# Performance work log

Measured on AMD Instinct MI355X. Metric: run time of the kernel, lower is better.

Reference implementation:

```python
import jax, jax.numpy as jnp
import numpy as np

D_MODEL = 512
N_HEADS = 4
D_HEAD = D_MODEL // N_HEADS
D_FF = 2048
N_LAYERS = 3
IN_DIM = 25
OUT_DIM = 1
PRE = 20          # pre_training_size
SCALE = 10.0      # scaling_factor
EPS = 1e-5


def setup_inputs() -> dict:
    key = jax.random.key(0)
    ks = jax.random.split(key, 20)
    B, S = 4, 2048
    def gn(k, shape, fan_in):
        return jax.random.normal(k, shape, jnp.float32) * (1.0 / np.sqrt(fan_in))
    return {
        "src": jax.random.normal(ks[0], (B, S, IN_DIM), jnp.float32),
        "emb_w": gn(ks[1], (D_MODEL, IN_DIM), IN_DIM),
        "emb_b": jnp.zeros((D_MODEL,), jnp.float32),
        "in_w": gn(ks[2], (N_LAYERS, 3 * D_MODEL, D_MODEL), D_MODEL),
        "in_b": jnp.zeros((N_LAYERS, 3 * D_MODEL), jnp.float32),
        "out_w": gn(ks[3], (N_LAYERS, D_MODEL, D_MODEL), D_MODEL),
        "out_b": jnp.zeros((N_LAYERS, D_MODEL), jnp.float32),
        "ln1_g": jnp.ones((N_LAYERS, D_MODEL), jnp.float32),
        "ln1_b": jnp.zeros((N_LAYERS, D_MODEL), jnp.float32),
        "ln2_g": jnp.ones((N_LAYERS, D_MODEL), jnp.float32),
        "ln2_b": jnp.zeros((N_LAYERS, D_MODEL), jnp.float32),
        "ff1_w": gn(ks[4], (N_LAYERS, D_FF, D_MODEL), D_MODEL),
        "ff1_b": jnp.zeros((N_LAYERS, D_FF), jnp.float32),
        "ff2_w": gn(ks[5], (N_LAYERS, D_MODEL, D_FF), D_FF),
        "ff2_b": jnp.zeros((N_LAYERS, D_MODEL), jnp.float32),
        "dec_w": gn(ks[6], (OUT_DIM, D_MODEL), D_MODEL),
        "dec_b": jnp.zeros((OUT_DIM,), jnp.float32),
    }


def _layer_norm(x, g, b):
    mu = jnp.mean(x, axis=-1, keepdims=True)
    var = jnp.var(x, axis=-1, keepdims=True)
    return (x - mu) * jax.lax.rsqrt(var + EPS) * g + b


def _pos_encoding(seq_len):
    # eval mode: start index 0, no dropout
    pos = jnp.arange(seq_len, dtype=jnp.float32)[:, None]           # [S,1]
    div = jnp.exp(jnp.arange(0, D_MODEL, 2, dtype=jnp.float32) * (-np.log(10000.0) / D_MODEL))  # [D/2]
    ang = pos * div                                                  # [S,D/2]
    return jnp.stack([jnp.sin(ang), jnp.cos(ang)], axis=-1).reshape(seq_len, D_MODEL)


def _causal_mask(seq_len):
    row = jnp.arange(seq_len)[:, None]
    col = jnp.arange(seq_len)[None, :]
    mask = jnp.where(col <= row, 0.0, -jnp.inf).astype(jnp.float32)
    # include_training_period=True: first PRE x PRE block unmasked
    return mask.at[:PRE, :PRE].set(0.0)


def reference(src, emb_w, emb_b, in_w, in_b, out_w, out_b,
              ln1_g, ln1_b, ln2_g, ln2_b, ff1_w, ff1_b, ff2_w, ff2_b,
              dec_w, dec_b):
    B, S, _ = src.shape
    x = src @ emb_w.T + emb_b                    # [B,S,D]
    x = x + _pos_encoding(S)[None]
    mask = _causal_mask(S)                       # [S,S]
    scale = 1.0 / np.sqrt(D_HEAD)
    for l in range(N_LAYERS):
        # --- self-attention (post-norm, eager bmm+softmax+bmm path) ---
        qkv = x @ in_w[l].T + in_b[l]            # [B,S,3D]
        q, k, v = jnp.split(qkv, 3, axis=-1)
        q = q.reshape(B, S, N_HEADS, D_HEAD).transpose(0, 2, 1, 3)
        k = k.reshape(B, S, N_HEADS, D_HEAD).transpose(0, 2, 1, 3)
        v = v.reshape(B, S, N_HEADS, D_HEAD).transpose(0, 2, 1, 3)
        scores = jnp.einsum('bhqd,bhkd->bhqk', q, k) * scale + mask
        attn = jax.nn.softmax(scores, axis=-1)   # [B,H,S,S] (need_weights=True path)
        o = jnp.einsum('bhqk,bhkd->bhqd', attn, v)
        o = o.transpose(0, 2, 1, 3).reshape(B, S, D_MODEL)
        o = o @ out_w[l].T + out_b[l]
        x = _layer_norm(x + o, ln1_g[l], ln1_b[l])
        # --- FFN ---
        h = jax.nn.relu(x @ ff1_w[l].T + ff1_b[l])
        h = h @ ff2_w[l].T + ff2_b[l]
        x = _layer_norm(x + h, ln2_g[l], ln2_b[l])
    out = jnp.tanh(x @ dec_w.T + dec_b) * SCALE  # [B,S,1]
    return out
```

## Files before the change

kernel.cpp:

```cpp
#include <hip/hip_runtime.h>

#define S_LEN 2048
#define DMODEL 512

typedef __attribute__((ext_vector_type(8))) short bf16x8;
typedef __attribute__((ext_vector_type(4))) float f32x4;
typedef __attribute__((ext_vector_type(4))) unsigned short u16x4;
typedef __attribute__((ext_vector_type(8))) unsigned short u16x8;
typedef __attribute__((ext_vector_type(2))) unsigned int u32x2;

__device__ __forceinline__ unsigned short f2bf(float f) {
    unsigned int u = __float_as_uint(f);
    u += 0x7fff + ((u >> 16) & 1);
    return (unsigned short)(u >> 16);
}
__device__ __forceinline__ float bf2f(unsigned short h) {
    return __uint_as_float(((unsigned int)h) << 16);
}
__device__ __forceinline__ void gll16(const void* g, void* l) {
    __builtin_amdgcn_global_load_lds(
        (const __attribute__((address_space(1))) unsigned int*)g,
        (__attribute__((address_space(3))) unsigned int*)l, 16, 0, 0);
}

__global__ __launch_bounds__(256) void conv_all(
    const float4* __restrict__ in_w, const float4* __restrict__ out_w,
    const float4* __restrict__ ff1_w, const float4* __restrict__ ff2_w,
    u16x4* __restrict__ in_wb, u16x4* __restrict__ out_wb,
    u16x4* __restrict__ ff1_wb, u16x4* __restrict__ ff2_wb)
{
    int i = blockIdx.x * 256 + threadIdx.x;
    const float4* src; u16x4* dst; int j;
    if (i < 589824)        { src = in_w;  dst = in_wb;  j = i; }
    else if (i < 786432)   { src = out_w; dst = out_wb; j = i - 589824; }
    else if (i < 1572864)  { src = ff1_w; dst = ff1_wb; j = i - 786432; }
    else                   { src = ff2_w; dst = ff2_wb; j = i - 1572864; }
    float4 v = src[j];
    u16x4 o = { f2bf(v.x), f2bf(v.y), f2bf(v.z), f2bf(v.w) };
    dst[j] = o;
}

__global__ __launch_bounds__(256) void embed_kernel(
    const float* __restrict__ src, const float* __restrict__ ew,
    const float* __restrict__ eb, float* __restrict__ X,
    unsigned short* __restrict__ Xb)
{
    int rid = blockIdx.x;
    int s = rid & (S_LEN - 1);
    int tid = threadIdx.x;
    __shared__ float sr[25];
    if (tid < 25) sr[tid] = src[rid * 25 + tid];
    __syncthreads();
    #pragma unroll
    for (int rep = 0; rep < 2; rep++) {
        int d = tid + rep * 256;
        float a = eb[d];
        #pragma unroll
        for (int k = 0; k < 25; k++) a = fmaf(sr[k], ew[d * 25 + k], a);
        int i2 = d & ~1;
        float div = expf(-(float)i2 * (9.210340371976184f / 512.f));
        float ang = (float)s * div;
        a += (d & 1) ? cosf(ang) : sinf(ang);
        X[(size_t)rid * DMODEL + d] = a;
        Xb[(size_t)rid * DMODEL + d] = f2bf(a);
    }
}

template<int MODE, int BN>
__global__ __launch_bounds__(256) void gemm_bf16(
    const unsigned short* __restrict__ A, int lda,
    const unsigned short* __restrict__ W, int K,
    const float* __restrict__ bias,
    unsigned short* __restrict__ out, int ldc,
    unsigned short* __restrict__ out2)
{
    constexpr int NJ = BN / 32;
    __shared__ __align__(16) unsigned short As[128 * 64];
    __shared__ __align__(16) unsigned short Ws[BN * 64];
    int tid = threadIdx.x;
    int lane = tid & 63, w = tid >> 6;
    int g = lane >> 4, c15 = lane & 15;
    int wm = w >> 1, wn = w & 1;
    int bm, bn;
    if (BN == 64) {
        int raw = blockIdx.x;
        int lid = ((raw & 7) << 6) | (raw >> 3);
        bn = lid & 7; bm = lid >> 3;
    } else {
        bm = blockIdx.y; bn = blockIdx.x;
    }

    f32x4 acc[4][NJ];
    #pragma unroll
    for (int i = 0; i < 4; i++)
        #pragma unroll
        for (int j = 0; j < NJ; j++) acc[i][j] = (f32x4){0.f, 0.f, 0.f, 0.f};

    const int nk = K >> 6;
    for (int kk = 0; kk < nk; kk++) {
        __syncthreads();
        #pragma unroll
        for (int i = 0; i < 4; i++) {
            int chunk = tid + i * 256;
            int r = chunk >> 3, c = chunk & 7;
            int cs = c ^ (r & 7);
            gll16(A + (size_t)(bm * 128 + r) * lda + kk * 64 + cs * 8,
                  (void*)(As + chunk * 8));
        }
        #pragma unroll
        for (int i = 0; i < BN / 32; i++) {
            int chunk = tid + i * 256;
            int r = chunk >> 3, c = chunk & 7;
            int cs = c ^ (r & 7);
            gll16(W + (size_t)(bn * BN + r) * K + kk * 64 + cs * 8,
                  (void*)(Ws + chunk * 8));
        }
        __syncthreads();
        bf16x8 a[4][2], b[NJ][2];
        #pragma unroll
        for (int mi = 0; mi < 4; mi++) {
            int row = wm * 64 + mi * 16 + c15;
            #pragma unroll
            for (int h = 0; h < 2; h++) {
                int ck = (h * 4 + g) ^ (row & 7);
                a[mi][h] = *(const bf16x8*)((const char*)As + row * 128 + ck * 16);
            }
        }
        #pragma unroll
        for (int nj = 0; nj < NJ; nj++) {
            int row = wn * (BN / 2) + nj * 16 + c15;
            #pragma unroll
            for (int h = 0; h < 2; h++) {
                int ck = (h * 4 + g) ^ (row & 7);
                b[nj][h] = *(const bf16x8*)((const char*)Ws + row * 128 + ck * 16);
            }
        }
        __builtin_amdgcn_s_setprio(1);
        #pragma unroll
        for (int h = 0; h < 2; h++)
            #pragma unroll
            for (int mi = 0; mi < 4; mi++)
                #pragma unroll
                for (int nj = 0; nj < NJ; nj++)
                    acc[mi][nj] = __builtin_amdgcn_mfma_f32_16x16x32_bf16(
                        a[mi][h], b[nj][h], acc[mi][nj], 0, 0, 0);
        __builtin_amdgcn_s_setprio(0);
    }
    #pragma unroll
    for (int nj = 0; nj < NJ; nj++) {
        int colb = bn * BN + wn * (BN / 2) + nj * 16;
        float bv = bias[colb + c15];
        #pragma unroll
        for (int mi = 0; mi < 4; mi++) {
            int rowb = bm * 128 + wm * 64 + mi * 16 + g * 4;
            if (MODE == 3 && colb >= 1024) {
                int cv = colb - 1024 + c15;
                int hh = cv >> 7, d = cv & 127;
                int bb = rowb >> 11, t = rowb & (S_LEN - 1);
                u16x4 pk;
                #pragma unroll
                for (int r = 0; r < 4; r++) pk[r] = f2bf(acc[mi][nj][r] + bv);
                *(u16x4*)(out2 + ((size_t)(bb * 4 + hh) * 128 + d) * S_LEN + t) = pk;
            } else {
                #pragma unroll
                for (int r = 0; r < 4; r++) {
                    float v = acc[mi][nj][r] + bv;
                    if (MODE == 2) v = fmaxf(v, 0.f);
                    out[(size_t)(rowb + r) * ldc + colb + c15] = f2bf(v);
                }
            }
        }
    }
}

__global__ __launch_bounds__(256) void flash_attn(
    const unsigned short* __restrict__ QKb,
    const unsigned short* __restrict__ Vt,
    unsigned short* __restrict__ Ob,
    unsigned short* __restrict__ Opart,
    float* __restrict__ Mpart,
    float* __restrict__ Lpart)
{
    __shared__ __align__(16) unsigned short Ks[2][32 * 128];
    __shared__ __align__(16) unsigned short Vts[2][128 * 32];
    __shared__ __align__(16) unsigned short Plds[4][16 * 40];
    const float scale = 0.08838834764831845f;
    int tid = threadIdx.x;
    int lane = tid & 63, w = tid >> 6;
    int g = lane >> 4, c15 = lane & 15;
    int raw = blockIdx.x;
    int lid = (raw & 7) * 96 + (raw >> 3);
    int bh = lid / 48, idx = lid - bh * 48;
    int b = bh >> 2, h = bh & 3;
    int qb, kt0, nkt, split;
    if (idx < 16) { qb = idx; kt0 = 0; nkt = 2 * qb + 2; split = -1; }
    else {
        int s = idx - 16;
        qb = 16 + (s >> 1);
        int j = s & 1;
        kt0 = j * (qb + 1);
        nkt = qb + 1;
        split = bh * 32 + (qb - 16) * 2 + j;
    }

    bf16x8 q[4];
    {
        const unsigned short* qrow =
            QKb + (size_t)(b * S_LEN + qb * 64 + w * 16 + c15) * 1024 + h * 128;
        #pragma unroll
        for (int k0 = 0; k0 < 4; k0++) q[k0] = *(const bf16x8*)(qrow + k0 * 32 + g * 8);
    }
    f32x4 o[8];
    #pragma unroll
    for (int cd = 0; cd < 8; cd++) o[cd] = (f32x4){0.f, 0.f, 0.f, 0.f};
    float m = -3e38f, l = 0.f;

    auto stage = [&](int kt, int bi) {
        #pragma unroll
        for (int i = 0; i < 2; i++) {
            int chunk = tid + i * 256;
            int r = chunk >> 4, c = chunk & 15;
            int cs = (c & 8) | ((c ^ r) & 7);
            gll16(QKb + (size_t)(b * S_LEN + kt * 32 + r) * 1024 + 512 + h * 128 + cs * 8,
                  (void*)(Ks[bi] + chunk * 8));
        }
        #pragma unroll
        for (int i = 0; i < 2; i++) {
            int chunk = tid + i * 256;
            int r = chunk >> 2, c = chunk & 3;
            int cs = (c ^ r) & 3;
            gll16(Vt + ((size_t)(b * 4 + h) * 128 + r) * S_LEN + kt * 32 + cs * 8,
                  (void*)(Vts[bi] + chunk * 8));
        }
    };

    stage(kt0, 0);
    __syncthreads();
    int buf = 0;

    for (int t = 0; t < nkt; t++) {
        int kt = kt0 + t;
        if (t + 1 < nkt) stage(kt + 1, buf ^ 1);
        f32x4 sf[2];
        __builtin_amdgcn_s_setprio(1);
        #pragma unroll
        for (int c = 0; c < 2; c++) {
            sf[c] = (f32x4){0.f, 0.f, 0.f, 0.f};
            int tok16 = c * 16 + c15;
            #pragma unroll
            for (int k0 = 0; k0 < 4; k0++) {
                int ck = k0 * 4 + g;
                int cs = (ck & 8) | ((ck ^ tok16) & 7);
                bf16x8 kf = *(const bf16x8*)((const char*)Ks[buf] + tok16 * 256 + cs * 16);
                sf[c] = __builtin_amdgcn_mfma_f32_16x16x32_bf16(kf, q[k0], sf[c], 0, 0, 0);
            }
        }
        __builtin_amdgcn_s_setprio(0);
        if (kt >= 2 * qb) {
            int qr = qb * 64 + w * 16 + c15;
            #pragma unroll
            for (int c = 0; c < 2; c++)
                #pragma unroll
                for (int r = 0; r < 4; r++) {
                    int tok = kt * 32 + c * 16 + g * 4 + r;
                    bool ok = (tok <= qr) || (qr < 20 && tok < 20);
                    if (!ok) sf[c][r] = -3e38f;
                }
        }
        float t0 = fmaxf(fmaxf(sf[0][0], sf[0][1]), fmaxf(sf[0][2], sf[0][3]));
        float t1 = fmaxf(fmaxf(sf[1][0], sf[1][1]), fmaxf(sf[1][2], sf[1][3]));
        float mt = fmaxf(t0, t1);
        mt = fmaxf(mt, __shfl_xor(mt, 16));
        mt = fmaxf(mt, __shfl_xor(mt, 32));
        bool need = !__all(mt <= m + 90.5f);
        float sc = 1.f;
        if (need) {
            float mn = fmaxf(m, mt);
            sc = __expf((m - mn) * scale);
            m = mn;
        }
        float msc = m * scale;
        #pragma unroll
        for (int c = 0; c < 2; c++)
            #pragma unroll
            for (int r = 0; r < 4; r++)
                sf[c][r] = __expf(fmaf(sf[c][r], scale, -msc));
        float s0 = (sf[0][0] + sf[0][1]) + (sf[0][2] + sf[0][3]);
        float s1 = (sf[1][0] + sf[1][1]) + (sf[1][2] + sf[1][3]);
        float ls = s0 + s1;
        ls += __shfl_xor(ls, 16);
        ls += __shfl_xor(ls, 32);
        if (need) l *= sc;
        l += ls;
        #pragma unroll
        for (int c = 0; c < 2; c++) {
            unsigned int lo = ((unsigned int)f2bf(sf[c][1]) << 16) | f2bf(sf[c][0]);
            unsigned int hi = ((unsigned int)f2bf(sf[c][3]) << 16) | f2bf(sf[c][2]);
            u32x2 pk = {lo, hi};
            *(u32x2*)&Plds[w][c15 * 40 + c * 16 + g * 4] = pk;
        }
        if (need) {
            float r0 = __shfl(sc, g * 4 + 0);
            float r1 = __shfl(sc, g * 4 + 1);
            float r2 = __shfl(sc, g * 4 + 2);
            float r3 = __shfl(sc, g * 4 + 3);
            #pragma unroll
            for (int cd = 0; cd < 8; cd++) {
                o[cd][0] *= r0; o[cd][1] *= r1; o[cd][2] *= r2; o[cd][3] *= r3;
            }
        }
        bf16x8 pa = *(const bf16x8*)((const char*)&Plds[w][0] + c15 * 80 + g * 16);
        __builtin_amdgcn_s_setprio(1);
        #pragma unroll
        for (int cd = 0; cd < 8; cd++) {
            int dv = cd * 16 + c15;
            int cs = (g ^ dv) & 3;
            bf16x8 vf = *(const bf16x8*)((const char*)Vts[buf] + dv * 64 + cs * 16);
            o[cd] = __builtin_amdgcn_mfma_f32_16x16x32_bf16(pa, vf, o[cd], 0, 0, 0);
        }
        __builtin_amdgcn_s_setprio(0);
        __syncthreads();
        buf ^= 1;
    }

    if (split < 0) {
        float li0 = 1.f / __shfl(l, g * 4 + 0);
        float li1 = 1.f / __shfl(l, g * 4 + 1);
        float li2 = 1.f / __shfl(l, g * 4 + 2);
        float li3 = 1.f / __shfl(l, g * 4 + 3);
        size_t obase = (size_t)(b * S_LEN + qb * 64 + w * 16 + g * 4) * 512 + h * 128;
        #pragma unroll
        for (int cd = 0; cd < 8; cd++) {
            Ob[obase + 0 * 512 + cd * 16 + c15] = f2bf(o[cd][0] * li0);
            Ob[obase + 1 * 512 + cd * 16 + c15] = f2bf(o[cd][1] * li1);
            Ob[obase + 2 * 512 + cd * 16 + c15] = f2bf(o[cd][2] * li2);
            Ob[obase + 3 * 512 + cd * 16 + c15] = f2bf(o[cd][3] * li3);
        }
    } else {
        unsigned short* op = Opart + (size_t)split * 8192;
        int rb = w * 16 + g * 4;
        #pragma unroll
        for (int cd = 0; cd < 8; cd++) {
            op[(rb + 0) * 128 + cd * 16 + c15] = f2bf(o[cd][0]);
            op[(rb + 1) * 128 + cd * 16 + c15] = f2bf(o[cd][1]);
            op[(rb + 2) * 128 + cd * 16 + c15] = f2bf(o[cd][2]);
            op[(rb + 3) * 128 + cd * 16 + c15] = f2bf(o[cd][3]);
        }
        if (g == 0) {
            Mpart[split * 64 + w * 16 + c15] = m;
            Lpart[split * 64 + w * 16 + c15] = l;
        }
    }
}

__global__ __launch_bounds__(256) void attn_merge(
    const unsigned short* __restrict__ Opart,
    const float* __restrict__ Mpart, const float* __restrict__ Lpart,
    unsigned short* __restrict__ Ob)
{
    const float scale = 0.08838834764831845f;
    int bid = blockIdx.x;
    int bh = bid >> 4, qe = bid & 15;
    int qb = 16 + qe;
    int b = bh >> 2, h = bh & 3;
    int p0 = bh * 32 + qe * 2;
    int t = threadIdx.x;
    int r = t >> 2, dq = t & 3;
    float m0 = Mpart[p0 * 64 + r], m1 = Mpart[(p0 + 1) * 64 + r];
    float l0 = Lpart[p0 * 64 + r], l1 = Lpart[(p0 + 1) * 64 + r];
    float ms = fmaxf(m0, m1);
    float w0 = __expf((m0 - ms) * scale), w1 = __expf((m1 - ms) * scale);
    float linv = 1.f / (l0 * w0 + l1 * w1);
    w0 *= linv; w1 *= linv;
    const unsigned short* o0 = Opart + (size_t)p0 * 8192 + r * 128 + dq * 32;
    const unsigned short* o1 = o0 + 8192;
    unsigned short* od = Ob + (size_t)(b * S_LEN + qb * 64 + r) * 512 + h * 128 + dq * 32;
    #pragma unroll
    for (int i = 0; i < 4; i++) {
        u16x8 a = *(const u16x8*)(o0 + i * 8);
        u16x8 c = *(const u16x8*)(o1 + i * 8);
        u16x8 d;
        #pragma unroll
        for (int j = 0; j < 8; j++)
            d[j] = f2bf(bf2f(a[j]) * w0 + bf2f(c[j]) * w1);
        *(u16x8*)(od + i * 8) = d;
    }
}

__global__ __launch_bounds__(256) void add_ln_kernel(
    float* __restrict__ X, const unsigned short* __restrict__ D,
    const float* __restrict__ gw, const float* __restrict__ bw,
    unsigned short* __restrict__ Xb)
{
    int row = blockIdx.x;
    int tid = threadIdx.x;
    size_t base = (size_t)row * DMODEL;
    float v0 = X[base + tid] + bf2f(D[base + tid]);
    float v1 = X[base + tid + 256] + bf2f(D[base + tid + 256]);
    float s = v0 + v1;
    float sq = v0 * v0 + v1 * v1;
    #pragma unroll
    for (int off = 32; off > 0; off >>= 1) {
        s  += __shfl_down(s, off);
        sq += __shfl_down(sq, off);
    }
    __shared__ float red[2][4];
    int wv = tid >> 6;
    if ((tid & 63) == 0) { red[0][wv] = s; red[1][wv] = sq; }
    __syncthreads();
    s  = red[0][0] + red[0][1] + red[0][2] + red[0][3];
    sq = red[1][0] + red[1][1] + red[1][2] + red[1][3];
    float mu = s * (1.f / DMODEL);
    float var = sq * (1.f / DMODEL) - mu * mu;
    float rs = rsqrtf(var + 1e-5f);
    float y0 = (v0 - mu) * rs * gw[tid] + bw[tid];
    float y1 = (v1 - mu) * rs * gw[tid + 256] + bw[tid + 256];
    X[base + tid] = y0;
    X[base + tid + 256] = y1;
    Xb[base + tid] = f2bf(y0);
    Xb[base + tid + 256] = f2bf(y1);
}

__global__ __launch_bounds__(256) void decoder_kernel(
    const float* __restrict__ X, const float* __restrict__ w,
    const float* __restrict__ bias, float* __restrict__ out)
{
    int tid = threadIdx.x;
    int lane = tid & 63;
    int row = blockIdx.x * 4 + (tid >> 6);
    float s = 0.f;
    size_t base = (size_t)row * DMODEL;
    #pragma unroll
    for (int i = 0; i < 8; i++) s = fmaf(X[base + lane + i * 64], w[lane + i * 64], s);
    #pragma unroll
    for (int off = 32; off > 0; off >>= 1) s += __shfl_down(s, off);
    if (lane == 0) out[row] = tanhf(s + bias[0]) * 10.0f;
}

extern "C" void kernel_launch(void* const* d_in, const int* in_sizes, int n_in,
                              void* d_out, int out_size, void* d_ws, size_t ws_size,
                              hipStream_t stream)
{
    const float* src   = (const float*)d_in[0];
    const float* emb_w = (const float*)d_in[1];
    const float* emb_b = (const float*)d_in[2];
    const float* in_w  = (const float*)d_in[3];
    const float* in_b  = (const float*)d_in[4];
    const float* out_w = (const float*)d_in[5];
    const float* out_b = (const float*)d_in[6];
    const float* ln1_g = (const float*)d_in[7];
    const float* ln1_b = (const float*)d_in[8];
    const float* ln2_g = (const float*)d_in[9];
    const float* ln2_b = (const float*)d_in[10];
    const float* ff1_w = (const float*)d_in[11];
    const float* ff1_b = (const float*)d_in[12];
    const float* ff2_w = (const float*)d_in[13];
    const float* ff2_b = (const float*)d_in[14];
    const float* dec_w = (const float*)d_in[15];
    const float* dec_b = (const float*)d_in[16];

    char* ws = (char*)d_ws;
    float*          X   = (float*)ws;
    unsigned short* Xb  = (unsigned short*)(ws + (16u << 20));
    unsigned short* Pb  = (unsigned short*)(ws + (24u << 20));
    unsigned short* Ob  = (unsigned short*)(ws + (32u << 20));
    unsigned short* QKb = (unsigned short*)(ws + (40u << 20));
    unsigned short* Vt  = (unsigned short*)(ws + (56u << 20));
    unsigned short* Hb  = (unsigned short*)(ws + (40u << 20));
    unsigned short* Opart = (unsigned short*)(ws + (16u << 20));
    float* Mpart = (float*)(ws + (24u << 20));
    float* Lpart = Mpart + 512 * 64;
    unsigned short* in_wb  = (unsigned short*)(ws + (72u << 20));
    unsigned short* out_wb = in_wb  + 3u * 1536 * 512;
    unsigned short* ff1_wb = out_wb + 3u * 512 * 512;
    unsigned short* ff2_wb = ff1_wb + 3u * 2048 * 512;
    float* outp = (float*)d_out;
    const int M = 4 * S_LEN;

    conv_all<<<9216, 256, 0, stream>>>(
        (const float4*)in_w, (const float4*)out_w,
        (const float4*)ff1_w, (const float4*)ff2_w,
        (u16x4*)in_wb, (u16x4*)out_wb, (u16x4*)ff1_wb, (u16x4*)ff2_wb);

    embed_kernel<<<M, 256, 0, stream>>>(src, emb_w, emb_b, X, Xb);

    for (int l = 0; l < 3; l++) {
        gemm_bf16<3, 128><<<dim3(12, 64), 256, 0, stream>>>(
            Xb, 512, in_wb + (size_t)l * 1536 * 512, 512, in_b + l * 1536,
            QKb, 1024, Vt);
        flash_attn<<<768, 256, 0, stream>>>(QKb, Vt, Ob, Opart, Mpart, Lpart);
        attn_merge<<<256, 256, 0, stream>>>(Opart, Mpart, Lpart, Ob);
        gemm_bf16<1, 64><<<dim3(512), 256, 0, stream>>>(
            Ob, 512, out_wb + (size_t)l * 512 * 512, 512, out_b + l * 512,
            Pb, 512, nullptr);
        add_ln_kernel<<<M, 256, 0, stream>>>(X, Pb, ln1_g + l * 512, ln1_b + l * 512, Xb);
        gemm_bf16<2, 128><<<dim3(16, 64), 256, 0, stream>>>(
            Xb, 512, ff1_wb + (size_t)l * 2048 * 512, 512, ff1_b + l * 2048,
            Hb, 2048, nullptr);
        gemm_bf16<1, 64><<<dim3(512), 256, 0, stream>>>(
            Hb, 2048, ff2_wb + (size_t)l * 512 * 2048, 2048, ff2_b + l * 512,
            Pb, 512, nullptr);
        add_ln_kernel<<<M, 256, 0, stream>>>(X, Pb, ln2_g + l * 512, ln2_b + l * 512, Xb);
    }

    decoder_kernel<<<M / 4, 256, 0, stream>>>(X, dec_w, dec_b, outp);
}
```

Baseline: 564.8 us.

## Split more attention query blocks, precompute staging pointers, re-swizzle V tile

The causal-attention work split now divides every query block from 8 upward into two key ranges, not only blocks 16 and up. This raises the flash-attention grid from 768 to 896 blocks and the merge grid from 256 to 384, with the partial buffers moved and enlarged to match. The aim is to shorten the longest blocks and balance load across CUs. In exchange it writes and merges more partial outputs. Staging now advances precomputed global pointers instead of recomputing addresses each tile, and the V-tile LDS swizzle adds a row>>2 term to reduce bank conflicts.

```diff
diff --git a/kernel.cpp b/kernel.cpp
--- a/kernel.cpp
+++ b/kernel.cpp
@@ -189,18 +189,18 @@
     int lane = tid & 63, w = tid >> 6;
     int g = lane >> 4, c15 = lane & 15;
     int raw = blockIdx.x;
-    int lid = (raw & 7) * 96 + (raw >> 3);
-    int bh = lid / 48, idx = lid - bh * 48;
+    int lid = (raw & 7) * 112 + (raw >> 3);
+    int bh = lid / 56, idx = lid - bh * 56;
     int b = bh >> 2, h = bh & 3;
     int qb, kt0, nkt, split;
-    if (idx < 16) { qb = idx; kt0 = 0; nkt = 2 * qb + 2; split = -1; }
+    if (idx < 8) { qb = idx; kt0 = 0; nkt = 2 * qb + 2; split = -1; }
     else {
-        int s = idx - 16;
-        qb = 16 + (s >> 1);
+        int s = idx - 8;
+        qb = 8 + (s >> 1);
         int j = s & 1;
         kt0 = j * (qb + 1);
         nkt = qb + 1;
-        split = bh * 32 + (qb - 16) * 2 + j;
+        split = bh * 48 + (qb - 8) * 2 + j;
     }
 
     bf16x8 q[4];
@@ -215,32 +215,36 @@
     for (int cd = 0; cd < 8; cd++) o[cd] = (f32x4){0.f, 0.f, 0.f, 0.f};
     float m = -3e38f, l = 0.f;
 
-    auto stage = [&](int kt, int bi) {
-        #pragma unroll
-        for (int i = 0; i < 2; i++) {
-            int chunk = tid + i * 256;
-            int r = chunk >> 4, c = chunk & 15;
-            int cs = (c & 8) | ((c ^ r) & 7);
-            gll16(QKb + (size_t)(b * S_LEN + kt * 32 + r) * 1024 + 512 + h * 128 + cs * 8,
-                  (void*)(Ks[bi] + chunk * 8));
-        }
-        #pragma unroll
-        for (int i = 0; i < 2; i++) {
-            int chunk = tid + i * 256;
-            int r = chunk >> 2, c = chunk & 3;
-            int cs = (c ^ r) & 3;
-            gll16(Vt + ((size_t)(b * 4 + h) * 128 + r) * S_LEN + kt * 32 + cs * 8,
-                  (void*)(Vts[bi] + chunk * 8));
-        }
+    int rk0 = tid >> 4, ck = tid & 15;
+    int csk0 = (ck & 8) | ((ck ^ rk0) & 7);
+    int rk1 = rk0 + 16;
+    int csk1 = (ck & 8) | ((ck ^ rk1) & 7);
+    const unsigned short* kp0 = QKb + (size_t)(b * S_LEN + kt0 * 32 + rk0) * 1024 + 512 + h * 128 + csk0 * 8;
+    const unsigned short* kp1 = QKb + (size_t)(b * S_LEN + kt0 * 32 + rk1) * 1024 + 512 + h * 128 + csk1 * 8;
+    int rv0 = tid >> 2, cv = tid & 3;
+    int csv0 = cv ^ ((rv0 ^ (rv0 >> 2)) & 3);
+    int rv1 = rv0 + 64;
+    int csv1 = cv ^ ((rv1 ^ (rv1 >> 2)) & 3);
+    const unsigned short* VtB = Vt + (size_t)(b * 4 + h) * 128 * S_LEN;
+    const unsigned short* vp0 = VtB + (size_t)rv0 * S_LEN + kt0 * 32 + csv0 * 8;
+    const unsigned short* vp1 = VtB + (size_t)rv1 * S_LEN + kt0 * 32 + csv1 * 8;
+
+    auto stage = [&](int bi) {
+        gll16(kp0, (void*)(Ks[bi] + tid * 8));
+        gll16(kp1, (void*)(Ks[bi] + (tid + 256) * 8));
+        gll16(vp0, (void*)(Vts[bi] + tid * 8));
+        gll16(vp1, (void*)(Vts[bi] + (tid + 256) * 8));
+        kp0 += 32 * 1024; kp1 += 32 * 1024;
+        vp0 += 32; vp1 += 32;
     };
 
-    stage(kt0, 0);
+    stage(0);
     __syncthreads();
     int buf = 0;
 
     for (int t = 0; t < nkt; t++) {
         int kt = kt0 + t;
-        if (t + 1 < nkt) stage(kt + 1, buf ^ 1);
+        if (t + 1 < nkt) stage(buf ^ 1);
         f32x4 sf[2];
         __builtin_amdgcn_s_setprio(1);
         #pragma unroll
@@ -249,8 +253,8 @@
             int tok16 = c * 16 + c15;
             #pragma unroll
             for (int k0 = 0; k0 < 4; k0++) {
-                int ck = k0 * 4 + g;
-                int cs = (ck & 8) | ((ck ^ tok16) & 7);
+                int ck2 = k0 * 4 + g;
+                int cs = (ck2 & 8) | ((ck2 ^ tok16) & 7);
                 bf16x8 kf = *(const bf16x8*)((const char*)Ks[buf] + tok16 * 256 + cs * 16);
                 sf[c] = __builtin_amdgcn_mfma_f32_16x16x32_bf16(kf, q[k0], sf[c], 0, 0, 0);
             }
@@ -314,7 +318,7 @@
         #pragma unroll
         for (int cd = 0; cd < 8; cd++) {
             int dv = cd * 16 + c15;
-            int cs = (g ^ dv) & 3;
+            int cs = g ^ ((dv ^ (dv >> 2)) & 3);
             bf16x8 vf = *(const bf16x8*)((const char*)Vts[buf] + dv * 64 + cs * 16);
             o[cd] = __builtin_amdgcn_mfma_f32_16x16x32_bf16(pa, vf, o[cd], 0, 0, 0);
         }
@@ -360,10 +364,10 @@
 {
     const float scale = 0.08838834764831845f;
     int bid = blockIdx.x;
-    int bh = bid >> 4, qe = bid & 15;
-    int qb = 16 + qe;
+    int bh = bid / 24, qe = bid - bh * 24;
+    int qb = 8 + qe;
     int b = bh >> 2, h = bh & 3;
-    int p0 = bh * 32 + qe * 2;
+    int p0 = bh * 48 + qe * 2;
     int t = threadIdx.x;
     int r = t >> 2, dq = t & 3;
     float m0 = Mpart[p0 * 64 + r], m1 = Mpart[(p0 + 1) * 64 + r];
@@ -468,8 +472,8 @@
     unsigned short* Vt  = (unsigned short*)(ws + (56u << 20));
     unsigned short* Hb  = (unsigned short*)(ws + (40u << 20));
     unsigned short* Opart = (unsigned short*)(ws + (16u << 20));
-    float* Mpart = (float*)(ws + (24u << 20));
-    float* Lpart = Mpart + 512 * 64;
+    float* Mpart = (float*)(ws + (28u << 20));
+    float* Lpart = Mpart + 768 * 64;
     unsigned short* in_wb  = (unsigned short*)(ws + (72u << 20));
     unsigned short* out_wb = in_wb  + 3u * 1536 * 512;
     unsigned short* ff1_wb = out_wb + 3u * 512 * 512;
@@ -488,8 +492,8 @@
         gemm_bf16<3, 128><<<dim3(12, 64), 256, 0, stream>>>(
             Xb, 512, in_wb + (size_t)l * 1536 * 512, 512, in_b + l * 1536,
             QKb, 1024, Vt);
-        flash_attn<<<768, 256, 0, stream>>>(QKb, Vt, Ob, Opart, Mpart, Lpart);
-        attn_merge<<<256, 256, 0, stream>>>(Opart, Mpart, Lpart, Ob);
+        flash_attn<<<896, 256, 0, stream>>>(QKb, Vt, Ob, Opart, Mpart, Lpart);
+        attn_merge<<<384, 256, 0, stream>>>(Opart, Mpart, Lpart, Ob);
         gemm_bf16<1, 64><<<dim3(512), 256, 0, stream>>>(
             Ob, 512, out_wb + (size_t)l * 512 * 512, 512, out_b + l * 512,
             Pb, 512, nullptr);
```

Measured after the change: 595.5 us. +5.4%, slower.
